# Performance work log

Measured on AMD Instinct MI355X. Metric: run time of the kernel, lower is better.

Reference implementation:

```python
import jax, jax.numpy as jnp
import numpy as np

N_NODES = 100000
N_HEDGES = 25000
NNZ = 1600000
IN_CH = 128
HEADS_OUT = 128  # heads * out_channels = 8 * 16


def setup_inputs() -> dict:
    key = jax.random.key(0)
    k1, k2, k3, k4, k5, k6 = jax.random.split(key, 6)
    X = jax.random.normal(k1, (N_NODES, IN_CH), dtype=jnp.float32)
    Wlin = jax.random.normal(k2, (IN_CH, HEADS_OUT), dtype=jnp.float32) * (1.0 / np.sqrt(IN_CH))
    degE = jax.random.uniform(k3, (N_HEDGES, 1), dtype=jnp.float32)
    degV = jax.random.uniform(k4, (N_NODES, 1), dtype=jnp.float32)
    W = jnp.ones((N_HEDGES, 1), dtype=jnp.float32)
    g1_src = jax.random.randint(k5, (NNZ,), 0, N_NODES, dtype=jnp.int32)
    g1_dst = jax.random.randint(k6, (NNZ,), 0, N_HEDGES, dtype=jnp.int32)
    return {"X": X, "Wlin": Wlin, "degE": degE, "degV": degV, "W": W,
            "g1_src": g1_src, "g1_dst": g1_dst}


def reference(X, Wlin, degE, degV, W, g1_src, g1_dst):
    # Linear projection (no bias): [N, in_ch] @ [in_ch, heads*out] -> [N, HO]
    Xp = X @ Wlin
    # Stage 1: copy_u_sum over g1 (node -> hyperedge): out[e] = sum_{v in e} Xp[v]
    Xe = jax.ops.segment_sum(Xp[g1_src], g1_dst, num_segments=N_HEDGES)
    # Elementwise hyperedge scaling: degE then W (W is ones buffer in original)
    Xe = Xe * degE * W
    # Stage 2: copy_u_sum over g2 = g1^T (hyperedge -> node)
    Xv = jax.ops.segment_sum(Xe[g1_dst], g1_src, num_segments=N_NODES)
    # Node degree scaling
    Xv = Xv * degV
    return Xv
```

## Files before the change

### kernel.cpp

```cpp
#include <hip/hip_runtime.h>
#include <hip/hip_bf16.h>


#define CAPE 128
#define CAPV 64
#define LDK  136
#define RW   6250
#define RW2  12500

typedef __attribute__((ext_vector_type(8))) short bf16x8;
typedef __attribute__((ext_vector_type(4))) float f32x4;
typedef __attribute__((ext_vector_type(8))) float f32x8;

__device__ __forceinline__ unsigned short f32_to_bf16(float f) {
    unsigned int u = __float_as_uint(f);
    u += 0x7FFFu + ((u >> 16) & 1u);
    return (unsigned short)(u >> 16);
}
__device__ __forceinline__ float bf16_to_f32(unsigned short h) {
    return __uint_as_float(((unsigned int)h) << 16);
}


__device__ __forceinline__ void scan_body(unsigned char* __restrict__ h8, int n,
                                          int b, int nch, int* __restrict__ cnt) {
    int run = 0;
    for (int c0 = 0; c0 < nch; c0 += 16) {
        unsigned char v[16];
#pragma unroll
        for (int j = 0; j < 16; ++j)
            v[j] = h8[(long)(c0 + j) * n + b];
        unsigned char w[16];
#pragma unroll
        for (int j = 0; j < 16; ++j) {
            w[j] = (unsigned char)run;
            run += v[j];
        }
#pragma unroll
        for (int j = 0; j < 16; ++j)
            h8[(long)(c0 + j) * n + b] = w[j];
    }
    cnt[b] = run;
}

__device__ __forceinline__ void hist_body(unsigned int* __restrict__ s32,
                                          const int* __restrict__ key, int nnz,
                                          unsigned int* __restrict__ hist,
                                          int n4, int ch, int c, int w0, int w1,
                                          int tid) {
    const int nw = w1 - w0;
    for (int i = tid; i < nw; i += 256) s32[i] = 0;
    __syncthreads();
    int e0 = c * ch, e1 = e0 + ch; if (e1 > nnz) e1 = nnz;
    for (int e = e0 + tid; e < e1; e += 256) {
        int k = key[e];
        int w = k >> 2;
        if (w >= w0 && w < w1)
            atomicAdd(&s32[w - w0], 1u << ((k & 3) * 8));
    }
    __syncthreads();
    for (int i = tid; i < nw; i += 256)
        hist[(long)c * n4 + w0 + i] = s32[i];
}

__device__ __forceinline__ void gatherE_body(int id, int tid,
                                             const unsigned short* __restrict__ Xp,
                                             const int* __restrict__ cntE,
                                             const int* __restrict__ adjE,
                                             const float* __restrict__ degE,
                                             const float* __restrict__ Wbuf,
                                             unsigned short* __restrict__ Xe,
                                             int nE) {
    int t = id * 256 + tid;
    int e = t >> 4;
    if (e >= nE) return;
    int c = (t & 15) << 3;
    int len = cntE[e];
    if (len > CAPE) len = CAPE;
    const int* adj = adjE + (long)e * CAPE;
    float acc[8];
#pragma unroll
    for (int q = 0; q < 8; ++q) acc[q] = 0.f;

    int i = 0;
    for (; i + 8 <= len; i += 8) {
        int4 a0 = *(const int4*)(adj + i);
        int4 a1 = *(const int4*)(adj + i + 4);
        int v[8] = {a0.x, a0.y, a0.z, a0.w, a1.x, a1.y, a1.z, a1.w};
        bf16x8 h[8];
#pragma unroll
        for (int j = 0; j < 8; ++j)
            h[j] = *(const bf16x8*)(Xp + (long)v[j] * 128 + c);
#pragma unroll
        for (int j = 0; j < 8; ++j)
#pragma unroll
            for (int q = 0; q < 8; ++q)
                acc[q] += bf16_to_f32((unsigned short)h[j][q]);
    }
    for (; i + 4 <= len; i += 4) {
        int4 a0 = *(const int4*)(adj + i);
        int v[4] = {a0.x, a0.y, a0.z, a0.w};
        bf16x8 h[4];
#pragma unroll
        for (int j = 0; j < 4; ++j)
            h[j] = *(const bf16x8*)(Xp + (long)v[j] * 128 + c);
#pragma unroll
        for (int j = 0; j < 4; ++j)
#pragma unroll
            for (int q = 0; q < 8; ++q)
                acc[q] += bf16_to_f32((unsigned short)h[j][q]);
    }
    for (; i < len; ++i) {
        int v = adj[i];
        bf16x8 h = *(const bf16x8*)(Xp + (long)v * 128 + c);
#pragma unroll
        for (int q = 0; q < 8; ++q)
            acc[q] += bf16_to_f32((unsigned short)h[q]);
    }

    float sc = degE[e] * Wbuf[e];
    bf16x8 o;
#pragma unroll
    for (int q = 0; q < 8; ++q) o[q] = (short)f32_to_bf16(acc[q] * sc);
    *(bf16x8*)(Xe + (long)e * 128 + c) = o;
}


__global__ __launch_bounds__(256) void k_init(const float* __restrict__ Wl,
                                              unsigned short* __restrict__ Wt) {
    int idx = blockIdx.x * 256 + threadIdx.x;
    if (idx < 128 * 128) {
        int n = idx >> 7, k = idx & 127;
        Wt[idx] = f32_to_bf16(Wl[k * 128 + n]);
    }
}

__global__ __launch_bounds__(256) void k_gemm_histE(
    const float* __restrict__ X, const unsigned short* __restrict__ Wt,
    unsigned short* __restrict__ Xp, int nrows, int nGemm,
    const int* __restrict__ keyE, int nnz,
    unsigned int* __restrict__ histE32, int nE4, int che, int nchE)
{
    __shared__ union {
        struct { unsigned short Xs[64 * LDK]; unsigned short Wt[128 * LDK]; } g;
        unsigned int s32[RW];
    } sm;

    int bid = blockIdx.x;
    const int tid = threadIdx.x;

    if (bid < nGemm) {
        const int row0 = bid * 64;
        for (int base = tid * 4; base < 64 * 128; base += 1024) {
            int r = base >> 7, c = base & 127;
            float4 v = make_float4(0.f, 0.f, 0.f, 0.f);
            if (row0 + r < nrows) v = *(const float4*)(X + (long)(row0 + r) * 128 + c);
            ushort4 h;
            h.x = f32_to_bf16(v.x); h.y = f32_to_bf16(v.y);
            h.z = f32_to_bf16(v.z); h.w = f32_to_bf16(v.w);
            *(ushort4*)(sm.g.Xs + r * LDK + c) = h;
        }
        for (int base = tid * 4; base < 128 * 128; base += 1024) {
            int n = base >> 7, k = base & 127;
            ushort4 h = *(const ushort4*)(Wt + base);
            *(ushort4*)(sm.g.Wt + n * LDK + k) = h;
        }
        __syncthreads();

        const int w    = tid >> 6;
        const int lane = tid & 63;
        const int m    = lane & 15;
        const int quad = lane >> 4;

        f32x4 acc[8];
#pragma unroll
        for (int ct = 0; ct < 8; ++ct) acc[ct] = (f32x4){0.f, 0.f, 0.f, 0.f};

#pragma unroll
        for (int kk = 0; kk < 4; ++kk) {
            bf16x8 a = *(const bf16x8*)(sm.g.Xs + (w * 16 + m) * LDK + kk * 32 + quad * 8);
#pragma unroll
            for (int ct = 0; ct < 8; ++ct) {
                bf16x8 b = *(const bf16x8*)(sm.g.Wt + (ct * 16 + m) * LDK + kk * 32 + quad * 8);
                acc[ct] = __builtin_amdgcn_mfma_f32_16x16x32_bf16(a, b, acc[ct], 0, 0, 0);
            }
        }
#pragma unroll
        for (int ct = 0; ct < 8; ++ct) {
#pragma unroll
            for (int r = 0; r < 4; ++r) {
                int row = row0 + w * 16 + quad * 4 + r;
                if (row < nrows)
                    Xp[(long)row * 128 + ct * 16 + m] = f32_to_bf16(acc[ct][r]);
            }
        }
        return;
    }

    int c = bid - nGemm;
    if (c < nchE)
        hist_body(sm.s32, keyE, nnz, histE32, nE4, che, c, 0, nE4, tid);
}

__global__ __launch_bounds__(256) void k_scanE_histV(
    unsigned char* __restrict__ histE8, int* __restrict__ cntE,
    int nE, int nchE, int nScanE,
    const int* __restrict__ keyV, int nnz,
    unsigned int* __restrict__ histV32, int nV4, int chv, int nchV)
{
    __shared__ unsigned int s32[RW2];
    int bid = blockIdx.x;
    const int tid = threadIdx.x;
    if (bid < nScanE) {
        int t = bid * 256 + tid;
        if (t < nE) scan_body(histE8, nE, t, nchE, cntE);
        return;
    }
    bid -= nScanE;
    const int c = bid % nchV, r = bid / nchV;
    const int w0 = r * RW2;
    int w1 = w0 + RW2; if (w1 > nV4) w1 = nV4;
    hist_body(s32, keyV, nnz, histV32, nV4, chv, c, w0, w1, tid);
}

__global__ __launch_bounds__(256) void k_scatE_scanV(
    const int* __restrict__ src, const int* __restrict__ dst, int nnz,
    const unsigned char* __restrict__ histE8, int* __restrict__ adjE,
    int nE4, int che, int nchE,
    unsigned char* __restrict__ histV8, int* __restrict__ cntV, int nV, int nchV)
{
    __shared__ unsigned int c32[RW];
    int bid = blockIdx.x;
    const int tid = threadIdx.x;
    if (bid < nchE) {
        const int c = bid;
        const unsigned int* brow = (const unsigned int*)histE8 + (long)c * nE4;
        for (int i = tid; i < nE4; i += 256) c32[i] = brow[i];
        __syncthreads();
        int e0 = c * che, e1 = e0 + che; if (e1 > nnz) e1 = nnz;
        for (int e = e0 + tid; e < e1; e += 256) {
            int k = dst[e];
            int sh = (k & 3) * 8;
            unsigned int old = atomicAdd(&c32[k >> 2], 1u << sh);
            int slot = (old >> sh) & 0xFF;
            if (slot < CAPE) adjE[(long)k * CAPE + slot] = src[e];
        }
        return;
    }
    int t = (bid - nchE) * 256 + tid;
    if (t < nV) scan_body(histV8, nV, t, nchV, cntV);
}

__global__ __launch_bounds__(256) void k_gathE_scatV(
    const unsigned short* __restrict__ Xp, const int* __restrict__ cntE,
    const int* __restrict__ adjE, const float* __restrict__ degE,
    const float* __restrict__ Wbuf, unsigned short* __restrict__ Xe,
    int nE, int nGathE,
    const int* __restrict__ src, const int* __restrict__ dst, int nnz,
    const unsigned char* __restrict__ histV8, unsigned short* __restrict__ adjV,
    int nV4, int chv, int nchV)
{
    __shared__ unsigned int c32[RW2];
    int bid = blockIdx.x;
    const int tid = threadIdx.x;
    if (bid < nGathE) {
        gatherE_body(bid, tid, Xp, cntE, adjE, degE, Wbuf, Xe, nE);
        return;
    }
    bid -= nGathE;
    const int c = bid % nchV, r = bid / nchV;
    const int w0 = r * RW2;
    int w1 = w0 + RW2; if (w1 > nV4) w1 = nV4;
    const int nw = w1 - w0;
    const unsigned int* brow = (const unsigned int*)histV8 + (long)c * nV4 + w0;
    for (int i = tid; i < nw; i += 256) c32[i] = brow[i];
    __syncthreads();
    int e0 = c * chv, e1 = e0 + chv; if (e1 > nnz) e1 = nnz;
    for (int e = e0 + tid; e < e1; e += 256) {
        int k = src[e];
        int w = k >> 2;
        if (w < w0 || w >= w1) continue;
        int sh = (k & 3) * 8;
        unsigned int old = atomicAdd(&c32[w - w0], 1u << sh);
        int slot = (old >> sh) & 0xFF;
        if (slot < CAPV) adjV[(long)k * CAPV + slot] = (unsigned short)dst[e];
    }
}

__global__ __launch_bounds__(256) void k_gatherV(const unsigned short* __restrict__ Xe,
                                                 const int* __restrict__ cntV,
                                                 const unsigned short* __restrict__ adjV,
                                                 const float* __restrict__ degV,
                                                 float* __restrict__ out,
                                                 int nV) {
    int t = blockIdx.x * 256 + threadIdx.x;
    int v = t >> 4;
    if (v >= nV) return;
    int c = (t & 15) << 3;
    int len = cntV[v];
    if (len > CAPV) len = CAPV;
    const unsigned short* adj = adjV + (long)v * CAPV;
    float acc[8];
#pragma unroll
    for (int q = 0; q < 8; ++q) acc[q] = 0.f;

    int i = 0;
    for (; i + 8 <= len; i += 8) {
        ushort4 a0 = *(const ushort4*)(adj + i);
        ushort4 a1 = *(const ushort4*)(adj + i + 4);
        int e[8] = {a0.x, a0.y, a0.z, a0.w, a1.x, a1.y, a1.z, a1.w};
        bf16x8 h[8];
#pragma unroll
        for (int j = 0; j < 8; ++j)
            h[j] = *(const bf16x8*)(Xe + (long)e[j] * 128 + c);
#pragma unroll
        for (int j = 0; j < 8; ++j)
#pragma unroll
            for (int q = 0; q < 8; ++q)
                acc[q] += bf16_to_f32((unsigned short)h[j][q]);
    }
    for (; i + 4 <= len; i += 4) {
        ushort4 a0 = *(const ushort4*)(adj + i);
        int e[4] = {a0.x, a0.y, a0.z, a0.w};
        bf16x8 h[4];
#pragma unroll
        for (int j = 0; j < 4; ++j)
            h[j] = *(const bf16x8*)(Xe + (long)e[j] * 128 + c);
#pragma unroll
        for (int j = 0; j < 4; ++j)
#pragma unroll
            for (int q = 0; q < 8; ++q)
                acc[q] += bf16_to_f32((unsigned short)h[j][q]);
    }
    for (; i < len; ++i) {
        int e = adj[i];
        bf16x8 h = *(const bf16x8*)(Xe + (long)e * 128 + c);
#pragma unroll
        for (int q = 0; q < 8; ++q)
            acc[q] += bf16_to_f32((unsigned short)h[q]);
    }

    float sc = degV[v];
    f32x8 o;
#pragma unroll
    for (int q = 0; q < 8; ++q) o[q] = acc[q] * sc;
    *(f32x8*)(out + (long)v * 128 + c) = o;
}

__global__ __launch_bounds__(256) void zero_f4(float4* __restrict__ p, int n4) {
    int i = blockIdx.x * 256 + threadIdx.x;
    if (i < n4) p[i] = make_float4(0.f, 0.f, 0.f, 0.f);
}

__global__ __launch_bounds__(256) void gemm_xw_f32(const float* __restrict__ X,
                                                   const float* __restrict__ Wl,
                                                   float* __restrict__ Xp,
                                                   int nrows) {
    __shared__ float Xs[32 * 128];
    const int tid = threadIdx.x;
    const int row0 = blockIdx.x * 32;
    for (int i = tid * 4; i < 32 * 128; i += 256 * 4) {
        int r = row0 + (i >> 7);
        float4 v = make_float4(0.f, 0.f, 0.f, 0.f);
        if (r < nrows) v = *(const float4*)(X + (long)row0 * 128 + i);
        *(float4*)(Xs + i) = v;
    }
    __syncthreads();
    const int col = tid & 127;
    const int rg  = (tid >> 7) * 16;
    float acc[16];
#pragma unroll
    for (int r = 0; r < 16; ++r) acc[r] = 0.f;
    for (int k = 0; k < 128; k += 4) {
        const float w0 = Wl[(k + 0) * 128 + col];
        const float w1 = Wl[(k + 1) * 128 + col];
        const float w2 = Wl[(k + 2) * 128 + col];
        const float w3 = Wl[(k + 3) * 128 + col];
#pragma unroll
        for (int r = 0; r < 16; ++r) {
            float4 x = *(const float4*)(Xs + (rg + r) * 128 + k);
            acc[r] = fmaf(x.w, w3, fmaf(x.z, w2, fmaf(x.y, w1, fmaf(x.x, w0, acc[r]))));
        }
    }
#pragma unroll
    for (int r = 0; r < 16; ++r) {
        int row = row0 + rg + r;
        if (row < nrows) Xp[(long)row * 128 + col] = acc[r];
    }
}

__global__ __launch_bounds__(256) void scatter_to_hedges(const float* __restrict__ Xp,
                                                         const int* __restrict__ src,
                                                         const int* __restrict__ dst,
                                                         float* __restrict__ Xe,
                                                         int nnz) {
    int t = blockIdx.x * 256 + threadIdx.x;
    int e = t >> 5;
    if (e >= nnz) return;
    int c = (t & 31) << 2;
    int s = src[e], d = dst[e];
    float4 v = *(const float4*)(Xp + (long)s * 128 + c);
    float* o = Xe + (long)d * 128 + c;
    atomicAdd(o + 0, v.x); atomicAdd(o + 1, v.y);
    atomicAdd(o + 2, v.z); atomicAdd(o + 3, v.w);
}

__global__ __launch_bounds__(256) void scatter_to_nodes(const float* __restrict__ Xe,
                                                        const int* __restrict__ src,
                                                        const int* __restrict__ dst,
                                                        const float* __restrict__ degE,
                                                        const float* __restrict__ Wbuf,
                                                        const float* __restrict__ degV,
                                                        float* __restrict__ out,
                                                        int nnz) {
    int t = blockIdx.x * 256 + threadIdx.x;
    int e = t >> 5;
    if (e >= nnz) return;
    int c = (t & 31) << 2;
    int s = src[e], d = dst[e];
    float sc = degE[d] * Wbuf[d] * degV[s];
    float4 v = *(const float4*)(Xe + (long)d * 128 + c);
    float* o = out + (long)s * 128 + c;
    atomicAdd(o + 0, v.x * sc); atomicAdd(o + 1, v.y * sc);
    atomicAdd(o + 2, v.z * sc); atomicAdd(o + 3, v.w * sc);
}

extern "C" void kernel_launch(void* const* d_in, const int* in_sizes, int n_in,
                              void* d_out, int out_size, void* d_ws, size_t ws_size,
                              hipStream_t stream) {
    const float* X    = (const float*)d_in[0];
    const float* Wlin = (const float*)d_in[1];
    const float* degE = (const float*)d_in[2];
    const float* degV = (const float*)d_in[3];
    const float* Wbuf = (const float*)d_in[4];
    const int* g1_src = (const int*)d_in[5];
    const int* g1_dst = (const int*)d_in[6];

    const int nE  = in_sizes[2];
    const int nV  = in_sizes[3];
    const int nnz = in_sizes[5];

    float* out = (float*)d_out;
    char* ws = (char*)d_ws;

    auto layout_size = [&](int cE, int cV) -> size_t {
        size_t o = 0;
        o += (size_t)nE * CAPE * 4;
        o += (size_t)nV * CAPV * 2;
        o += (size_t)nE * 4 + (size_t)nV * 4;
        size_t he = (size_t)cE * nE;
        size_t xe = (size_t)nE * 128 * 2;
        o += (he > xe) ? he : xe;
        o += (size_t)cV * nV;
        o += 128 * 128 * 2;
        o += 4096;
        return o;
    };

    int nchE = 256, nchV = 256;
    if (layout_size(nchE, nchV) > ws_size) { nchE = 256; nchV = 128; }
    if (layout_size(nchE, nchV) > ws_size) { nchE = 128; nchV = 128; }
    if (layout_size(nchE, nchV) > ws_size) { nchE = 64;  nchV = 64;  }

    const int nE4 = nE >> 2, nV4 = nV >> 2;
    const bool eligible = ((nE & 3) == 0) && ((nV & 3) == 0) && (nE4 <= RW) &&
                          layout_size(nchE, nchV) <= ws_size;

    if (eligible) {
        size_t boff = 0;
        auto alloc = [&](size_t bytes) -> char* {
            char* p = ws + boff;
            boff += (bytes + 255) & ~(size_t)255;
            return p;
        };
        int* adjE            = (int*)alloc((size_t)nE * CAPE * 4);
        unsigned short* adjV = (unsigned short*)alloc((size_t)nV * CAPV * 2);
        int* cntE            = (int*)alloc((size_t)nE * 4);
        int* cntV            = (int*)alloc((size_t)nV * 4);
        size_t he = (size_t)nchE * nE;
        size_t xe = (size_t)nE * 128 * 2;
        char* region1         = alloc((he > xe) ? he : xe);
        unsigned char* histE8 = (unsigned char*)region1;
        unsigned short* Xe    = (unsigned short*)region1;
        unsigned char* histV8 = (unsigned char*)alloc((size_t)nchV * nV);
        unsigned short* Wt    = (unsigned short*)alloc((size_t)128 * 128 * 2);

        unsigned short* Xp_bf = (unsigned short*)d_out;

        const int nrV = (nV4 + RW2 - 1) / RW2;
        const int che = (nnz + nchE - 1) / nchE;
        const int chv = (nnz + nchV - 1) / nchV;

        k_init<<<64, 256, 0, stream>>>(Wlin, Wt);

        int nGemm = (nV + 63) / 64;
        k_gemm_histE<<<nGemm + nchE, 256, 0, stream>>>(
            X, Wt, Xp_bf, nV, nGemm,
            g1_dst, nnz, (unsigned int*)histE8, nE4, che, nchE);

        int nScanE = (nE + 255) / 256;
        k_scanE_histV<<<nScanE + nchV * nrV, 256, 0, stream>>>(
            histE8, cntE, nE, nchE, nScanE,
            g1_src, nnz, (unsigned int*)histV8, nV4, chv, nchV);

        int nScanV = (nV + 255) / 256;
        k_scatE_scanV<<<nchE + nScanV, 256, 0, stream>>>(
            g1_src, g1_dst, nnz, histE8, adjE, nE4, che, nchE,
            histV8, cntV, nV, nchV);

        int nGathE = (nE * 16 + 255) / 256;
        k_gathE_scatV<<<nGathE + nchV * nrV, 256, 0, stream>>>(
            Xp_bf, cntE, adjE, degE, Wbuf, Xe, nE, nGathE,
            g1_src, g1_dst, nnz, histV8, adjV, nV4, chv, nchV);

        int gV = (nV * 16 + 255) / 256;
        k_gatherV<<<gV, 256, 0, stream>>>(Xe, cntV, adjV, degV, out, nV);
    } else {
        float* XeF = (float*)d_ws;
        float* Xp  = out;
        int n4 = nE * 128 / 4;
        zero_f4<<<(n4 + 255) / 256, 256, 0, stream>>>((float4*)XeF, n4);
        gemm_xw_f32<<<(nV + 31) / 32, 256, 0, stream>>>(X, Wlin, Xp, nV);
        long th = (long)nnz * 32;
        scatter_to_hedges<<<(int)((th + 255) / 256), 256, 0, stream>>>(Xp, g1_src, g1_dst,
                                                                       XeF, nnz);
        int m4 = out_size / 4;
        zero_f4<<<(m4 + 255) / 256, 256, 0, stream>>>((float4*)out, m4);
        scatter_to_nodes<<<(int)((th + 255) / 256), 256, 0, stream>>>(XeF, g1_src, g1_dst,
                                                                      degE, Wbuf, degV,
                                                                      out, nnz);
    }
}
```

Baseline: 327.4 us.

## Split node-side scatter into halves and overlap second half with node gather

Halves the node-range window size (RW2→RW) for the node histogram and scatter kernels, which lowers LDS use per block and doubles the number of row ranges. The node-side adjacency scatter is split in two. The first half runs alongside the hyperedge gather, and the second half runs alongside the node gather for nodes already finished by the first half. A trailing kernel gathers the remaining nodes. The aim is to overlap the serialized scatter with gather work, at the cost of each scatter block rescanning the full edge chunk for more row ranges.

```diff
diff --git a/kernel.cpp b/kernel.cpp
--- a/kernel.cpp
+++ b/kernel.cpp
@@ -6,7 +6,6 @@
 #define CAPV 64
 #define LDK  136
 #define RW   6250
-#define RW2  12500
 
 typedef __attribute__((ext_vector_type(8))) short bf16x8;
 typedef __attribute__((ext_vector_type(4))) float f32x4;
@@ -61,6 +60,30 @@
     __syncthreads();
     for (int i = tid; i < nw; i += 256)
         hist[(long)c * n4 + w0 + i] = s32[i];
+}
+
+__device__ __forceinline__ void scatV_body(unsigned int* __restrict__ c32,
+                                           const int* __restrict__ src,
+                                           const int* __restrict__ dst, int nnz,
+                                           const unsigned char* __restrict__ histV8,
+                                           unsigned short* __restrict__ adjV,
+                                           int nV4, int chv, int c, int r, int tid) {
+    const int w0 = r * RW;
+    int w1 = w0 + RW; if (w1 > nV4) w1 = nV4;
+    const int nw = w1 - w0;
+    const unsigned int* brow = (const unsigned int*)histV8 + (long)c * nV4 + w0;
+    for (int i = tid; i < nw; i += 256) c32[i] = brow[i];
+    __syncthreads();
+    int e0 = c * chv, e1 = e0 + chv; if (e1 > nnz) e1 = nnz;
+    for (int e = e0 + tid; e < e1; e += 256) {
+        int k = src[e];
+        int w = k >> 2;
+        if (w < w0 || w >= w1) continue;
+        int sh = (k & 3) * 8;
+        unsigned int old = atomicAdd(&c32[w - w0], 1u << sh);
+        int slot = (old >> sh) & 0xFF;
+        if (slot < CAPV) adjV[(long)k * CAPV + slot] = (unsigned short)dst[e];
+    }
 }
 
 __device__ __forceinline__ void gatherE_body(int id, int tid,
@@ -125,6 +148,67 @@
     *(bf16x8*)(Xe + (long)e * 128 + c) = o;
 }
 
+__device__ __forceinline__ void gatherV_body(int id, int tid,
+                                             const unsigned short* __restrict__ Xe,
+                                             const int* __restrict__ cntV,
+                                             const unsigned short* __restrict__ adjV,
+                                             const float* __restrict__ degV,
+                                             float* __restrict__ out,
+                                             int vLo, int vHi) {
+    int t = id * 256 + tid;
+    int v = vLo + (t >> 4);
+    if (v >= vHi) return;
+    int c = (t & 15) << 3;
+    int len = cntV[v];
+    if (len > CAPV) len = CAPV;
+    const unsigned short* adj = adjV + (long)v * CAPV;
+    float acc[8];
+#pragma unroll
+    for (int q = 0; q < 8; ++q) acc[q] = 0.f;
+
+    int i = 0;
+    for (; i + 8 <= len; i += 8) {
+        ushort4 a0 = *(const ushort4*)(adj + i);
+        ushort4 a1 = *(const ushort4*)(adj + i + 4);
+        int e[8] = {a0.x, a0.y, a0.z, a0.w, a1.x, a1.y, a1.z, a1.w};
+        bf16x8 h[8];
+#pragma unroll
+        for (int j = 0; j < 8; ++j)
+            h[j] = *(const bf16x8*)(Xe + (long)e[j] * 128 + c);
+#pragma unroll
+        for (int j = 0; j < 8; ++j)
+#pragma unroll
+            for (int q = 0; q < 8; ++q)
+                acc[q] += bf16_to_f32((unsigned short)h[j][q]);
+    }
+    for (; i + 4 <= len; i += 4) {
+        ushort4 a0 = *(const ushort4*)(adj + i);
+        int e[4] = {a0.x, a0.y, a0.z, a0.w};
+        bf16x8 h[4];
+#pragma unroll
+        for (int j = 0; j < 4; ++j)
+            h[j] = *(const bf16x8*)(Xe + (long)e[j] * 128 + c);
+#pragma unroll
+        for (int j = 0; j < 4; ++j)
+#pragma unroll
+            for (int q = 0; q < 8; ++q)
+                acc[q] += bf16_to_f32((unsigned short)h[j][q]);
+    }
+    for (; i < len; ++i) {
+        int e = adj[i];
+        bf16x8 h = *(const bf16x8*)(Xe + (long)e * 128 + c);
+#pragma unroll
+        for (int q = 0; q < 8; ++q)
+            acc[q] += bf16_to_f32((unsigned short)h[q]);
+    }
+
+    float sc = degV[v];
+    f32x8 o;
+#pragma unroll
+    for (int q = 0; q < 8; ++q) o[q] = acc[q] * sc;
+    *(f32x8*)(out + (long)v * 128 + c) = o;
+}
+
 
 __global__ __launch_bounds__(256) void k_init(const float* __restrict__ Wl,
                                               unsigned short* __restrict__ Wt) {
@@ -208,7 +292,7 @@
     const int* __restrict__ keyV, int nnz,
     unsigned int* __restrict__ histV32, int nV4, int chv, int nchV)
 {
-    __shared__ unsigned int s32[RW2];
+    __shared__ unsigned int s32[RW];
     int bid = blockIdx.x;
     const int tid = threadIdx.x;
     if (bid < nScanE) {
@@ -218,8 +302,8 @@
     }
     bid -= nScanE;
     const int c = bid % nchV, r = bid / nchV;
-    const int w0 = r * RW2;
-    int w1 = w0 + RW2; if (w1 > nV4) w1 = nV4;
+    const int w0 = r * RW;
+    int w1 = w0 + RW; if (w1 > nV4) w1 = nV4;
     hist_body(s32, keyV, nnz, histV32, nV4, chv, c, w0, w1, tid);
 }
 
@@ -260,7 +344,7 @@
     const unsigned char* __restrict__ histV8, unsigned short* __restrict__ adjV,
     int nV4, int chv, int nchV)
 {
-    __shared__ unsigned int c32[RW2];
+    __shared__ unsigned int c32[RW];
     int bid = blockIdx.x;
     const int tid = threadIdx.x;
     if (bid < nGathE) {
@@ -269,22 +353,27 @@
     }
     bid -= nGathE;
     const int c = bid % nchV, r = bid / nchV;
-    const int w0 = r * RW2;
-    int w1 = w0 + RW2; if (w1 > nV4) w1 = nV4;
-    const int nw = w1 - w0;
-    const unsigned int* brow = (const unsigned int*)histV8 + (long)c * nV4 + w0;
-    for (int i = tid; i < nw; i += 256) c32[i] = brow[i];
-    __syncthreads();
-    int e0 = c * chv, e1 = e0 + chv; if (e1 > nnz) e1 = nnz;
-    for (int e = e0 + tid; e < e1; e += 256) {
-        int k = src[e];
-        int w = k >> 2;
-        if (w < w0 || w >= w1) continue;
-        int sh = (k & 3) * 8;
-        unsigned int old = atomicAdd(&c32[w - w0], 1u << sh);
-        int slot = (old >> sh) & 0xFF;
-        if (slot < CAPV) adjV[(long)k * CAPV + slot] = (unsigned short)dst[e];
-    }
+    scatV_body(c32, src, dst, nnz, histV8, adjV, nV4, chv, c, r, tid);
+}
+
+__global__ __launch_bounds__(256) void k_gathV_scatV(
+    const unsigned short* __restrict__ Xe, const int* __restrict__ cntV,
+    const unsigned short* __restrict__ adjV, const float* __restrict__ degV,
+    float* __restrict__ out, int vSplit, int nGathV,
+    const int* __restrict__ src, const int* __restrict__ dst, int nnz,
+    const unsigned char* __restrict__ histV8, unsigned short* __restrict__ adjVw,
+    int nV4, int chv, int nchV, int rBase)
+{
+    __shared__ unsigned int c32[RW];
+    int bid = blockIdx.x;
+    const int tid = threadIdx.x;
+    if (bid < nGathV) {
+        gatherV_body(bid, tid, Xe, cntV, adjV, degV, out, 0, vSplit);
+        return;
+    }
+    bid -= nGathV;
+    const int c = bid % nchV, r = rBase + bid / nchV;
+    scatV_body(c32, src, dst, nnz, histV8, adjVw, nV4, chv, c, r, tid);
 }
 
 __global__ __launch_bounds__(256) void k_gatherV(const unsigned short* __restrict__ Xe,
@@ -292,59 +381,8 @@
                                                  const unsigned short* __restrict__ adjV,
                                                  const float* __restrict__ degV,
                                                  float* __restrict__ out,
-                                                 int nV) {
-    int t = blockIdx.x * 256 + threadIdx.x;
-    int v = t >> 4;
-    if (v >= nV) return;
-    int c = (t & 15) << 3;
-    int len = cntV[v];
-    if (len > CAPV) len = CAPV;
-    const unsigned short* adj = adjV + (long)v * CAPV;
-    float acc[8];
-#pragma unroll
-    for (int q = 0; q < 8; ++q) acc[q] = 0.f;
-
-    int i = 0;
-    for (; i + 8 <= len; i += 8) {
-        ushort4 a0 = *(const ushort4*)(adj + i);
-        ushort4 a1 = *(const ushort4*)(adj + i + 4);
-        int e[8] = {a0.x, a0.y, a0.z, a0.w, a1.x, a1.y, a1.z, a1.w};
-        bf16x8 h[8];
-#pragma unroll
-        for (int j = 0; j < 8; ++j)
-            h[j] = *(const bf16x8*)(Xe + (long)e[j] * 128 + c);
-#pragma unroll
-        for (int j = 0; j < 8; ++j)
-#pragma unroll
-            for (int q = 0; q < 8; ++q)
-                acc[q] += bf16_to_f32((unsigned short)h[j][q]);
-    }
-    for (; i + 4 <= len; i += 4) {
-        ushort4 a0 = *(const ushort4*)(adj + i);
-        int e[4] = {a0.x, a0.y, a0.z, a0.w};
-        bf16x8 h[4];
-#pragma unroll
-        for (int j = 0; j < 4; ++j)
-            h[j] = *(const bf16x8*)(Xe + (long)e[j] * 128 + c);
-#pragma unroll
-        for (int j = 0; j < 4; ++j)
-#pragma unroll
-            for (int q = 0; q < 8; ++q)
-                acc[q] += bf16_to_f32((unsigned short)h[j][q]);
-    }
-    for (; i < len; ++i) {
-        int e = adj[i];
-        bf16x8 h = *(const bf16x8*)(Xe + (long)e * 128 + c);
-#pragma unroll
-        for (int q = 0; q < 8; ++q)
-            acc[q] += bf16_to_f32((unsigned short)h[q]);
-    }
-
-    float sc = degV[v];
-    f32x8 o;
-#pragma unroll
-    for (int q = 0; q < 8; ++q) o[q] = acc[q] * sc;
-    *(f32x8*)(out + (long)v * 128 + c) = o;
+                                                 int vLo, int vHi) {
+    gatherV_body(blockIdx.x, threadIdx.x, Xe, cntV, adjV, degV, out, vLo, vHi);
 }
 
 __global__ __launch_bounds__(256) void zero_f4(float4* __restrict__ p, int n4) {
@@ -487,7 +525,9 @@
 
         unsigned short* Xp_bf = (unsigned short*)d_out;
 
-        const int nrV = (nV4 + RW2 - 1) / RW2;
+        const int nrV    = (nV4 + RW - 1) / RW;
+        const int rSplit = (nrV + 1) / 2;
+        int vSplit = rSplit * RW * 4; if (vSplit > nV) vSplit = nV;
         const int che = (nnz + nchE - 1) / nchE;
         const int chv = (nnz + nchV - 1) / nchV;
 
@@ -509,12 +549,20 @@
             histV8, cntV, nV, nchV);
 
         int nGathE = (nE * 16 + 255) / 256;
-        k_gathE_scatV<<<nGathE + nchV * nrV, 256, 0, stream>>>(
+        k_gathE_scatV<<<nGathE + nchV * rSplit, 256, 0, stream>>>(
             Xp_bf, cntE, adjE, degE, Wbuf, Xe, nE, nGathE,
             g1_src, g1_dst, nnz, histV8, adjV, nV4, chv, nchV);
 
-        int gV = (nV * 16 + 255) / 256;
-        k_gatherV<<<gV, 256, 0, stream>>>(Xe, cntV, adjV, degV, out, nV);
+        int nGathV1 = (vSplit * 16 + 255) / 256;
+        k_gathV_scatV<<<nGathV1 + nchV * (nrV - rSplit), 256, 0, stream>>>(
+            Xe, cntV, adjV, degV, out, vSplit, nGathV1,
+            g1_src, g1_dst, nnz, histV8, adjV, nV4, chv, nchV, rSplit);
+
+        if (vSplit < nV) {
+            int nGathV2 = ((nV - vSplit) * 16 + 255) / 256;
+            k_gatherV<<<nGathV2, 256, 0, stream>>>(Xe, cntV, adjV, degV, out,
+                                                   vSplit, nV);
+        }
     } else {
         float* XeF = (float*)d_ws;
         float* Xp  = out;
```

Result: slower. 341.0 us (+4.2%).
